# Kernel optimization log

Hardware: AMD Instinct MI355X
Metric: run time of the kernel (lower is better)

The kernel has to match this reference:

```python
import jax, jax.numpy as jnp
import numpy as np

N, E, D, H, ED = 50000, 400000, 64, 4, 16
C = D  # out_channels per head (GATv2Conv(model_dim, model_dim, ...))


def setup_inputs() -> dict:
    key = jax.random.key(0)
    ks = jax.random.split(key, 24)
    sD = 1.0 / np.sqrt(D)
    sE = 1.0 / np.sqrt(ED)
    sC = 1.0 / np.sqrt(C)
    inp = {
        "h": jax.random.normal(ks[0], (N, D), jnp.float32),
        "edge_index": jax.random.randint(ks[1], (2, E), 0, N, dtype=jnp.int32),
        "edge_attr": jax.random.normal(ks[2], (E, ED), jnp.float32),
    }
    for i, name in enumerate(["g1", "g2"]):
        b = 3 + i * 9
        inp[f"{name}_Wl"] = jax.random.normal(ks[b], (D, H * C), jnp.float32) * sD
        inp[f"{name}_bl"] = jax.random.normal(ks[b + 1], (H * C,), jnp.float32) * 0.02
        inp[f"{name}_Wr"] = jax.random.normal(ks[b + 2], (D, H * C), jnp.float32) * sD
        inp[f"{name}_br"] = jax.random.normal(ks[b + 3], (H * C,), jnp.float32) * 0.02
        inp[f"{name}_We"] = jax.random.normal(ks[b + 4], (ED, H * C), jnp.float32) * sE
        inp[f"{name}_att"] = jax.random.normal(ks[b + 5], (H, C), jnp.float32) * sC
        inp[f"{name}_bias"] = jax.random.normal(ks[b + 6], (C,), jnp.float32) * 0.02
        inp[f"ln{i+1}_g"] = jnp.ones((D,), jnp.float32)
        inp[f"ln{i+1}_b"] = jnp.zeros((D,), jnp.float32)
    return inp


def _layer_norm(x, g, b):
    mu = jnp.mean(x, axis=-1, keepdims=True)
    var = jnp.mean((x - mu) ** 2, axis=-1, keepdims=True)
    return (x - mu) * jax.lax.rsqrt(var + 1e-5) * g + b


def _gatv2(h, src, dst, edge_attr, Wl, bl, Wr, br, We, att, bias):
    # PyG GATv2Conv, concat=False, negative_slope=0.2, aggregation at dst
    xl = (h @ Wl + bl).reshape(N, H, C)  # source transform
    xr = (h @ Wr + br).reshape(N, H, C)  # target transform
    ez = (edge_attr @ We).reshape(E, H, C)
    x = jax.nn.leaky_relu(xl[src] + xr[dst] + ez, negative_slope=0.2)  # [E,H,C]
    alpha = jnp.einsum('ehc,hc->eh', x, att)  # attention logits per edge/head
    amax = jax.ops.segment_max(alpha, dst, num_segments=N)
    amax = jnp.where(jnp.isfinite(amax), amax, 0.0)
    ex = jnp.exp(alpha - amax[dst])
    denom = jax.ops.segment_sum(ex, dst, num_segments=N)
    a = ex / (denom[dst] + 1e-16)  # segment softmax over incoming edges
    out = jax.ops.segment_sum(xl[src] * a[..., None], dst, num_segments=N)  # [N,H,C]
    return jnp.mean(out, axis=1) + bias  # concat=False -> head mean, then bias


def reference(h, edge_index, edge_attr,
              g1_Wl, g1_bl, g1_Wr, g1_br, g1_We, g1_att, g1_bias, ln1_g, ln1_b,
              g2_Wl, g2_bl, g2_Wr, g2_br, g2_We, g2_att, g2_bias, ln2_g, ln2_b):
    src, dst = edge_index[0], edge_index[1]
    identity = h
    x = _gatv2(h, src, dst, edge_attr, g1_Wl, g1_bl, g1_Wr, g1_br, g1_We, g1_att, g1_bias)
    x = jax.nn.gelu(_layer_norm(x, ln1_g, ln1_b), approximate=False)
    x = _gatv2(x, src, dst, edge_attr, g2_Wl, g2_bl, g2_Wr, g2_br, g2_We, g2_att, g2_bias)
    x = _layer_norm(x, ln2_g, ln2_b)
    return jax.nn.gelu(x + identity, approximate=False)
```

## Files before the change

### kernel.cpp

```cpp
#include <hip/hip_runtime.h>
#include <math.h>

#define NN  50000
#define EE  400000
#define DD  64
#define HH  4
#define HC  256
#define EDD 16
#define CAPE 96

typedef _Float16 half_t;
typedef _Float16 h2 __attribute__((ext_vector_type(2)));

__device__ __forceinline__ float gelu_exact(float x) {
    return 0.5f * x * (1.0f + erff(x * 0.70710678118654752440f));
}
__device__ __forceinline__ float fast_exp(float x) {
    return __builtin_amdgcn_exp2f(x * 1.44269504088896340736f);
}

template <int CTRL>
__device__ __forceinline__ float dpp_add(float x) {
    const int t = __builtin_amdgcn_update_dpp(0, __float_as_int(x), CTRL, 0xF, 0xF, true);
    return x + __int_as_float(t);
}
__device__ __forceinline__ float row_sum16(float x) {
    x = dpp_add<0x128>(x);
    x = dpp_add<0x124>(x);
    x = dpp_add<0x122>(x);
    x = dpp_add<0x121>(x);
    return x;
}

__global__ void fill_u32(unsigned* __restrict__ p, unsigned v, int n) {
    int i = blockIdx.x * blockDim.x + threadIdx.x;
    int s = gridDim.x * blockDim.x;
    for (; i < n; i += s) p[i] = v;
}

__global__ void hist_k(const int* __restrict__ ei, int* __restrict__ deg) {
    int e = blockIdx.x * 256 + threadIdx.x;
    if (e < EE) atomicAdd(&deg[ei[EE + e]], 1);
}
__global__ void scan1_k(const int* __restrict__ deg, int* __restrict__ rowptr,
                        int* __restrict__ bsum) {
    __shared__ int s[256];
    int t = threadIdx.x, i = blockIdx.x * 256 + t;
    int v = (i < NN) ? deg[i] : 0;
    s[t] = v; __syncthreads();
    for (int o = 1; o < 256; o <<= 1) {
        int u = (t >= o) ? s[t - o] : 0;
        __syncthreads();
        s[t] += u;
        __syncthreads();
    }
    if (i < NN) rowptr[i] = s[t] - v;
    if (t == 255) bsum[blockIdx.x] = s[255];
}
__global__ void scan3_k(int* __restrict__ rowptr, const int* __restrict__ bsum,
                        int* __restrict__ cursor, int nb) {
    __shared__ int s[256];
    int t = threadIdx.x;
    int v = (t < nb) ? bsum[t] : 0;
    s[t] = v; __syncthreads();
    for (int o = 1; o < 256; o <<= 1) {
        int u = (t >= o) ? s[t - o] : 0;
        __syncthreads();
        s[t] += u;
        __syncthreads();
    }
    const int add = (blockIdx.x > 0) ? s[blockIdx.x - 1] : 0;
    int i = blockIdx.x * 256 + t;
    if (i < NN) {
        int r = rowptr[i] + add;
        rowptr[i] = r;
        cursor[i] = r;
    }
    if (i == 0) rowptr[NN] = EE;
}
__global__ void scatter_k(const int* __restrict__ ei, int* __restrict__ cursor,
                          const float* __restrict__ ea,
                          int* __restrict__ srcs, half_t* __restrict__ ea_h) {
    int e = blockIdx.x * 256 + threadIdx.x;
    if (e >= EE) return;
    int dst = ei[EE + e];
    int pos = atomicAdd(&cursor[dst], 1);
    srcs[pos] = ei[e];
    const float* s = ea + (long)e * EDD;
    half_t tmp[EDD];
#pragma unroll
    for (int k = 0; k < EDD; k++) tmp[k] = (half_t)s[k];
    int4* d = (int4*)(ea_h + (long)pos * EDD);
    d[0] = *(const int4*)&tmp[0];
    d[1] = *(const int4*)&tmp[8];
}

__global__ void wrange_k(const int* __restrict__ rowptr, int* __restrict__ wstart,
                         int* __restrict__ srcs, int nw, int cpe) {
    int w = blockIdx.x * 256 + threadIdx.x;
    if (blockIdx.x == 0 && threadIdx.x < 16) srcs[EE + threadIdx.x] = 0;
    if (w > nw) return;
    if (w == nw) { wstart[nw] = NN; return; }
    const int lo = w * cpe;
    int l = 0, r = NN;
    while (l < r) { int m = (l + r) >> 1; if (rowptr[m] >= lo) r = m; else l = m + 1; }
    wstart[w] = l;
}

__global__ __launch_bounds__(256) void gemm_node_lr(
    const float* __restrict__ X,
    const float* __restrict__ Wl, const float* __restrict__ bl,
    const float* __restrict__ Wr, const float* __restrict__ br,
    float* __restrict__ Yl, float* __restrict__ Yr)
{
    __shared__ half_t xs[32][64];
    const int tid  = threadIdx.x;
    const int col  = tid;
    const int base = blockIdx.x * 32;

#pragma unroll
    for (int i = 0; i < 2; i++) {
        const int f   = tid + i * 256;
        const int r   = f >> 4;
        const int row = base + r;
        const int rr  = (row < NN) ? row : (NN - 1);
        const float4 v = *(const float4*)(X + (long)rr * 64 + ((f & 15) << 2));
        h2 p0; p0.x = (half_t)v.x; p0.y = (half_t)v.y;
        h2 p1; p1.x = (half_t)v.z; p1.y = (half_t)v.w;
        int2 w;
        w.x = __builtin_bit_cast(int, p0);
        w.y = __builtin_bit_cast(int, p1);
        *(int2*)&xs[r][(f & 15) << 2] = w;
    }

    int wlp[32], wrp[32];
#pragma unroll
    for (int kk = 0; kk < 32; kk++) {
        h2 a;
        a.x = (half_t)Wl[(2 * kk)     * 256 + col];
        a.y = (half_t)Wl[(2 * kk + 1) * 256 + col];
        wlp[kk] = __builtin_bit_cast(int, a);
        h2 b;
        b.x = (half_t)Wr[(2 * kk)     * 256 + col];
        b.y = (half_t)Wr[(2 * kk + 1) * 256 + col];
        wrp[kk] = __builtin_bit_cast(int, b);
    }
    const float bbl = bl[col];
    const float bbr = br[col];

    __syncthreads();

#pragma unroll 2
    for (int r = 0; r < 32; r++) {
        const int row = base + r;
        float l0 = 0.f, l1 = 0.f, l2 = 0.f, l3 = 0.f;
        float r0 = 0.f, r1 = 0.f, r2 = 0.f, r3 = 0.f;
#pragma unroll
        for (int q = 0; q < 8; q++) {
            const int4 blk = *(const int4*)&xs[r][q << 3];
            const int* pr = (const int*)&blk;
            l0 = __builtin_amdgcn_fdot2(__builtin_bit_cast(h2, pr[0]),
                                        __builtin_bit_cast(h2, wlp[q * 4 + 0]), l0, false);
            l1 = __builtin_amdgcn_fdot2(__builtin_bit_cast(h2, pr[1]),
                                        __builtin_bit_cast(h2, wlp[q * 4 + 1]), l1, false);
            l2 = __builtin_amdgcn_fdot2(__builtin_bit_cast(h2, pr[2]),
                                        __builtin_bit_cast(h2, wlp[q * 4 + 2]), l2, false);
            l3 = __builtin_amdgcn_fdot2(__builtin_bit_cast(h2, pr[3]),
                                        __builtin_bit_cast(h2, wlp[q * 4 + 3]), l3, false);
            r0 = __builtin_amdgcn_fdot2(__builtin_bit_cast(h2, pr[0]),
                                        __builtin_bit_cast(h2, wrp[q * 4 + 0]), r0, false);
            r1 = __builtin_amdgcn_fdot2(__builtin_bit_cast(h2, pr[1]),
                                        __builtin_bit_cast(h2, wrp[q * 4 + 1]), r1, false);
            r2 = __builtin_amdgcn_fdot2(__builtin_bit_cast(h2, pr[2]),
                                        __builtin_bit_cast(h2, wrp[q * 4 + 2]), r2, false);
            r3 = __builtin_amdgcn_fdot2(__builtin_bit_cast(h2, pr[3]),
                                        __builtin_bit_cast(h2, wrp[q * 4 + 3]), r3, false);
        }
        if (row < NN) {
            Yl[(long)row * 256 + col] = (l0 + l1) + (l2 + l3) + bbl;
            Yr[(long)row * 256 + col] = (r0 + r1) + (r2 + r3) + bbr;
        }
    }
}

__device__ __forceinline__ float edge_part_dot2(const h2 ev[8], const int wpk[8][4],
                                                const float4 xlv, const float4 xrv,
                                                const float4 a4) {
    float e0 = 0.f, e1 = 0.f, e2 = 0.f, e3 = 0.f;
#pragma unroll
    for (int k = 0; k < 8; k++) {
        e0 = __builtin_amdgcn_fdot2(ev[k], __builtin_bit_cast(h2, wpk[k][0]), e0, false);
        e1 = __builtin_amdgcn_fdot2(ev[k], __builtin_bit_cast(h2, wpk[k][1]), e1, false);
        e2 = __builtin_amdgcn_fdot2(ev[k], __builtin_bit_cast(h2, wpk[k][2]), e2, false);
        e3 = __builtin_amdgcn_fdot2(ev[k], __builtin_bit_cast(h2, wpk[k][3]), e3, false);
    }
    float s0 = xlv.x + xrv.x + e0;
    float s1 = xlv.y + xrv.y + e1;
    float s2 = xlv.z + xrv.z + e2;
    float s3 = xlv.w + xrv.w + e3;
    s0 = (s0 > 0.f) ? s0 : 0.2f * s0;
    s1 = (s1 > 0.f) ? s1 : 0.2f * s1;
    s2 = (s2 > 0.f) ? s2 : 0.2f * s2;
    s3 = (s3 > 0.f) ? s3 : 0.2f * s3;
    return fmaf(s0, a4.x, fmaf(s1, a4.y, fmaf(s2, a4.z, s3 * a4.w)));
}

__global__ __launch_bounds__(256, 4) void fused_edge_node_k(
    const int* __restrict__ wstart,
    const int* __restrict__ rowptr, const int* __restrict__ srcs,
    const half_t* __restrict__ ea_h,
    const float* __restrict__ We, const float* __restrict__ att,
    const float* __restrict__ xl, const float* __restrict__ xr,
    const float* __restrict__ bias, const float* __restrict__ lng,
    const float* __restrict__ lnb, const float* __restrict__ identity,
    float* __restrict__ x1out, float* __restrict__ outp, int mode)
{
    __shared__ int4 eabuf[4][CAPE * 2];
    const int lane  = threadIdx.x & 63;
    const int wslot = threadIdx.x >> 6;
    const int h     = lane >> 4;
    const int jj    = lane & 15;
    const int gc    = (h << 6) + (jj << 2);
    const int c     = (jj << 2) + h;

    int wpk[8][4];
#pragma unroll
    for (int kk = 0; kk < 8; kk++) {
#pragma unroll
        for (int j = 0; j < 4; j++) {
            h2 t;
            t.x = (half_t)We[(2 * kk)     * HC + gc + j];
            t.y = (half_t)We[(2 * kk + 1) * HC + gc + j];
            wpk[kk][j] = __builtin_bit_cast(int, t);
        }
    }
#pragma unroll
    for (int kk = 0; kk < 8; kk++)
#pragma unroll
        for (int j = 0; j < 4; j++) asm volatile("" : "+v"(wpk[kk][j]));

    const float4 a4 = *(const float4*)(att + gc);
    const float bb  = bias[c];
    const float gg  = lng[c];
    const float cc  = lnb[c];

    const int wid  = blockIdx.x * 4 + wslot;
    const int nbeg = __builtin_amdgcn_readfirstlane(wstart[wid]);
    const int nend = __builtin_amdgcn_readfirstlane(wstart[wid + 1]);

    const int estart = __builtin_amdgcn_readfirstlane(rowptr[nbeg]);
    const int eend   = __builtin_amdgcn_readfirstlane(rowptr[nend]);
    {
        int nstage = eend - estart;
        if (nstage > CAPE) nstage = CAPE;
        const int4* __restrict__ gsrc = (const int4*)(ea_h + (long)estart * EDD);
        int4* l4 = &eabuf[wslot][0];
        for (int i = lane; i < nstage * 2; i += 64) l4[i] = gsrc[i];
    }

    int p0v = rowptr[nbeg];
    int p1v = rowptr[nbeg + 1];
    int sAn = srcs[p0v];
    int sBn = srcs[p0v + 1];

    for (int n = nbeg; n < nend; n++) {
        const int p0 = __builtin_amdgcn_readfirstlane(p0v);
        const int p1 = __builtin_amdgcn_readfirstlane(p1v);
        p0v = p1;
        p1v = rowptr[(n + 2 <= NN) ? (n + 2) : NN];
        int sA = sAn, sB = sBn;
        sAn = srcs[p1];
        sBn = srcs[p1 + 1];

        const float4 xrv = *(const float4*)(xr + (long)n * HC + gc);

        float dsum = 0.f;
        float ac0 = 0.f, ac1 = 0.f, ac2 = 0.f, ac3 = 0.f;

        int p = p0;
        for (; p + 1 < p1; p += 2) {
            const int srcA = __builtin_amdgcn_readfirstlane(sA);
            const int srcB = __builtin_amdgcn_readfirstlane(sB);
            sA = srcs[p + 2];
            sB = srcs[p + 3];

            const float4 xA = *(const float4*)(xl + (long)srcA * HC + gc);
            const float4 xB = *(const float4*)(xl + (long)srcB * HC + gc);

            int idx = p - estart;
            if (idx > CAPE - 2) idx = CAPE - 2;
            const int4* __restrict__ e4 = &eabuf[wslot][idx * 2];
            h2 evA[8], evB[8];
            *(int4*)&evA[0] = e4[0];  *(int4*)&evA[4] = e4[1];
            *(int4*)&evB[0] = e4[2];  *(int4*)&evB[4] = e4[3];

            float ptA = edge_part_dot2(evA, wpk, xA, xrv, a4);
            float ptB = edge_part_dot2(evB, wpk, xB, xrv, a4);

            ptA = row_sum16(ptA);
            ptB = row_sum16(ptB);

            const float wA = fast_exp(ptA);
            const float wB = fast_exp(ptB);
            dsum += (wA + wB);
            ac0 = fmaf(wA, xA.x, ac0); ac1 = fmaf(wA, xA.y, ac1);
            ac2 = fmaf(wA, xA.z, ac2); ac3 = fmaf(wA, xA.w, ac3);
            ac0 = fmaf(wB, xB.x, ac0); ac1 = fmaf(wB, xB.y, ac1);
            ac2 = fmaf(wB, xB.z, ac2); ac3 = fmaf(wB, xB.w, ac3);
        }

        if (p < p1) {
            const int src = __builtin_amdgcn_readfirstlane(sA);
            const float4 xv = *(const float4*)(xl + (long)src * HC + gc);
            int idx = p - estart;
            if (idx > CAPE - 1) idx = CAPE - 1;
            const int4* __restrict__ e4 = &eabuf[wslot][idx * 2];
            h2 ev[8];
            *(int4*)&ev[0] = e4[0];  *(int4*)&ev[4] = e4[1];
            float pt = edge_part_dot2(ev, wpk, xv, xrv, a4);
            pt = row_sum16(pt);
            const float w = fast_exp(pt);
            dsum += w;
            ac0 = fmaf(w, xv.x, ac0); ac1 = fmaf(w, xv.y, ac1);
            ac2 = fmaf(w, xv.z, ac2); ac3 = fmaf(w, xv.w, ac3);
        }

        const float inv = 1.0f / (dsum + 1e-16f);
        float v0 = ac0 * inv, v1 = ac1 * inv, v2 = ac2 * inv, v3 = ac3 * inv;

        v0 += __shfl_xor(v0, 16, 64); v0 += __shfl_xor(v0, 32, 64);
        v1 += __shfl_xor(v1, 16, 64); v1 += __shfl_xor(v1, 32, 64);
        v2 += __shfl_xor(v2, 16, 64); v2 += __shfl_xor(v2, 32, 64);
        v3 += __shfl_xor(v3, 16, 64); v3 += __shfl_xor(v3, 32, 64);

        float vv = (h == 0) ? v0 : (h == 1) ? v1 : (h == 2) ? v2 : v3;
        vv = vv * 0.25f + bb;

        float s = row_sum16(vv);
        s += __shfl_xor(s, 16, 64); s += __shfl_xor(s, 32, 64);
        const float mu = s * (1.0f / 64.0f);
        const float d  = vv - mu;
        float qv = row_sum16(d * d);
        qv += __shfl_xor(qv, 16, 64); qv += __shfl_xor(qv, 32, 64);
        const float rs = rsqrtf(qv * (1.0f / 64.0f) + 1e-5f);

        const float y = d * rs * gg + cc;
        if (mode == 0) {
            x1out[(long)n * DD + c] = gelu_exact(y);
        } else {
            const float id = identity[(long)n * DD + c];
            outp[(long)n * DD + c] = gelu_exact(y + id);
        }
    }
}

extern "C" void kernel_launch(void* const* d_in, const int* in_sizes, int n_in,
                              void* d_out, int out_size, void* d_ws, size_t ws_size,
                              hipStream_t stream) {
    (void)in_sizes; (void)n_in; (void)out_size; (void)ws_size;

    const float* h     = (const float*)d_in[0];
    const int*   ei    = (const int*)d_in[1];
    const float* ea    = (const float*)d_in[2];
    const float* g1Wl  = (const float*)d_in[3];
    const float* g1bl  = (const float*)d_in[4];
    const float* g1Wr  = (const float*)d_in[5];
    const float* g1br  = (const float*)d_in[6];
    const float* g1We  = (const float*)d_in[7];
    const float* g1att = (const float*)d_in[8];
    const float* g1bias= (const float*)d_in[9];
    const float* ln1g  = (const float*)d_in[10];
    const float* ln1b  = (const float*)d_in[11];
    const float* g2Wl  = (const float*)d_in[12];
    const float* g2bl  = (const float*)d_in[13];
    const float* g2Wr  = (const float*)d_in[14];
    const float* g2br  = (const float*)d_in[15];
    const float* g2We  = (const float*)d_in[16];
    const float* g2att = (const float*)d_in[17];
    const float* g2bias= (const float*)d_in[18];
    const float* ln2g  = (const float*)d_in[19];
    const float* ln2b  = (const float*)d_in[20];

    float* out = (float*)d_out;

    const int FUSED_BLOCKS = 4096;
    const int NW  = FUSED_BLOCKS * 4;
    const int CPE = (EE + NW - 1) / NW;

    float* ws = (float*)d_ws;
    size_t o = 0;
    float* xl     = ws + o;         o += 12800000;
    float* xr     = ws + o;         o += 12800000;
    float* x1     = ws + o;         o += 3200000;
    int*   rowptr = (int*)(ws + o); o += 50004;
    int*   deg    = (int*)(ws + o); o += 50000;
    int*   cursor = (int*)(ws + o); o += 50000;
    int*   bsum   = (int*)(ws + o); o += 256;
    int*   srcs   = (int*)(ws + o); o += 400016;
    int*   wstart = (int*)(ws + o); o += NW + 8;
    half_t* ea_h  = (half_t*)(ws + o); o += 3200064;

    const int GEMM_BLOCKS  = (NN + 31) / 32;
    const int SCAN_BLOCKS  = (NN + 255) / 256;
    const int EDGE_BLOCKS  = (EE + 255) / 256;
    const int WR_BLOCKS    = (NW + 1 + 255) / 256;

    fill_u32<<<256, 256, 0, stream>>>((unsigned*)deg, 0u, NN);
    hist_k<<<EDGE_BLOCKS, 256, 0, stream>>>(ei, deg);
    scan1_k<<<SCAN_BLOCKS, 256, 0, stream>>>(deg, rowptr, bsum);
    scan3_k<<<SCAN_BLOCKS, 256, 0, stream>>>(rowptr, bsum, cursor, SCAN_BLOCKS);
    wrange_k<<<WR_BLOCKS, 256, 0, stream>>>(rowptr, wstart, srcs, NW, CPE);
    scatter_k<<<EDGE_BLOCKS, 256, 0, stream>>>(ei, cursor, ea, srcs, ea_h);

    gemm_node_lr<<<GEMM_BLOCKS, 256, 0, stream>>>(h, g1Wl, g1bl, g1Wr, g1br, xl, xr);
    fused_edge_node_k<<<FUSED_BLOCKS, 256, 0, stream>>>(wstart, rowptr, srcs, ea_h,
                                                        g1We, g1att, xl, xr,
                                                        g1bias, ln1g, ln1b,
                                                        h, x1, out, 0);

    gemm_node_lr<<<GEMM_BLOCKS, 256, 0, stream>>>(x1, g2Wl, g2bl, g2Wr, g2br, xl, xr);
    fused_edge_node_k<<<FUSED_BLOCKS, 256, 0, stream>>>(wstart, rowptr, srcs, ea_h,
                                                        g2We, g2att, xl, xr,
                                                        g2bias, ln2g, ln2b,
                                                        h, x1, out, 1);
}
```

Measured before the change: 404.8 us.

## Merge CSR construction kernels into one cooperative kernel with grid syncs

Replaces six separate preprocessing launches (zero-fill, histogram, two scan passes, warp-range search, scatter) with one cooperative kernel of 1024 blocks that uses grid.sync between phases. The wrange search and the scatter now run in the same phase. The goal is to remove per-launch overhead and gaps between the small kernels. The cost is four grid-wide barriers, and the kernel depends on all 1024 blocks being co-resident for the cooperative launch.

```diff
diff --git a/kernel.cpp b/kernel.cpp
--- a/kernel.cpp
+++ b/kernel.cpp
@@ -1,4 +1,5 @@
 #include <hip/hip_runtime.h>
+#include <hip/hip_cooperative_groups.h>
 #include <math.h>
 
 #define NN  50000
@@ -32,79 +33,80 @@
     return x;
 }
 
-__global__ void fill_u32(unsigned* __restrict__ p, unsigned v, int n) {
-    int i = blockIdx.x * blockDim.x + threadIdx.x;
-    int s = gridDim.x * blockDim.x;
-    for (; i < n; i += s) p[i] = v;
-}
-
-__global__ void hist_k(const int* __restrict__ ei, int* __restrict__ deg) {
-    int e = blockIdx.x * 256 + threadIdx.x;
-    if (e < EE) atomicAdd(&deg[ei[EE + e]], 1);
-}
-__global__ void scan1_k(const int* __restrict__ deg, int* __restrict__ rowptr,
-                        int* __restrict__ bsum) {
+__global__ __launch_bounds__(256) void csr_coop_k(
+    const int* __restrict__ ei, const float* __restrict__ ea,
+    int* __restrict__ deg, int* __restrict__ rowptr, int* __restrict__ cursor,
+    int* __restrict__ bsum, int* __restrict__ srcs, half_t* __restrict__ ea_h,
+    int* __restrict__ wstart, int nw, int cpe)
+{
+    cooperative_groups::grid_group grid = cooperative_groups::this_grid();
     __shared__ int s[256];
-    int t = threadIdx.x, i = blockIdx.x * 256 + t;
-    int v = (i < NN) ? deg[i] : 0;
-    s[t] = v; __syncthreads();
-    for (int o = 1; o < 256; o <<= 1) {
-        int u = (t >= o) ? s[t - o] : 0;
-        __syncthreads();
-        s[t] += u;
-        __syncthreads();
-    }
-    if (i < NN) rowptr[i] = s[t] - v;
-    if (t == 255) bsum[blockIdx.x] = s[255];
-}
-__global__ void scan3_k(int* __restrict__ rowptr, const int* __restrict__ bsum,
-                        int* __restrict__ cursor, int nb) {
-    __shared__ int s[256];
-    int t = threadIdx.x;
-    int v = (t < nb) ? bsum[t] : 0;
-    s[t] = v; __syncthreads();
-    for (int o = 1; o < 256; o <<= 1) {
-        int u = (t >= o) ? s[t - o] : 0;
-        __syncthreads();
-        s[t] += u;
-        __syncthreads();
-    }
-    const int add = (blockIdx.x > 0) ? s[blockIdx.x - 1] : 0;
-    int i = blockIdx.x * 256 + t;
-    if (i < NN) {
-        int r = rowptr[i] + add;
-        rowptr[i] = r;
-        cursor[i] = r;
-    }
-    if (i == 0) rowptr[NN] = EE;
-}
-__global__ void scatter_k(const int* __restrict__ ei, int* __restrict__ cursor,
-                          const float* __restrict__ ea,
-                          int* __restrict__ srcs, half_t* __restrict__ ea_h) {
-    int e = blockIdx.x * 256 + threadIdx.x;
-    if (e >= EE) return;
-    int dst = ei[EE + e];
-    int pos = atomicAdd(&cursor[dst], 1);
-    srcs[pos] = ei[e];
-    const float* s = ea + (long)e * EDD;
-    half_t tmp[EDD];
-#pragma unroll
-    for (int k = 0; k < EDD; k++) tmp[k] = (half_t)s[k];
-    int4* d = (int4*)(ea_h + (long)pos * EDD);
-    d[0] = *(const int4*)&tmp[0];
-    d[1] = *(const int4*)&tmp[8];
-}
-
-__global__ void wrange_k(const int* __restrict__ rowptr, int* __restrict__ wstart,
-                         int* __restrict__ srcs, int nw, int cpe) {
-    int w = blockIdx.x * 256 + threadIdx.x;
-    if (blockIdx.x == 0 && threadIdx.x < 16) srcs[EE + threadIdx.x] = 0;
-    if (w > nw) return;
-    if (w == nw) { wstart[nw] = NN; return; }
-    const int lo = w * cpe;
-    int l = 0, r = NN;
-    while (l < r) { int m = (l + r) >> 1; if (rowptr[m] >= lo) r = m; else l = m + 1; }
-    wstart[w] = l;
+    const int tid  = blockIdx.x * 256 + threadIdx.x;
+    const int nthr = gridDim.x * 256;
+    const int nch  = (NN + 255) / 256;
+
+    for (int i = tid; i < NN; i += nthr) deg[i] = 0;
+    grid.sync();
+
+    for (int e = tid; e < EE; e += nthr) atomicAdd(&deg[ei[EE + e]], 1);
+    grid.sync();
+
+    if (blockIdx.x < nch) {
+        const int t = threadIdx.x, i = blockIdx.x * 256 + t;
+        const int v = (i < NN) ? deg[i] : 0;
+        s[t] = v; __syncthreads();
+        for (int o = 1; o < 256; o <<= 1) {
+            int u = (t >= o) ? s[t - o] : 0;
+            __syncthreads();
+            s[t] += u;
+            __syncthreads();
+        }
+        if (i < NN) rowptr[i] = s[t] - v;
+        if (t == 255) bsum[blockIdx.x] = s[255];
+    }
+    grid.sync();
+
+    if (blockIdx.x < nch) {
+        const int t = threadIdx.x;
+        const int v = (t < nch) ? bsum[t] : 0;
+        s[t] = v; __syncthreads();
+        for (int o = 1; o < 256; o <<= 1) {
+            int u = (t >= o) ? s[t - o] : 0;
+            __syncthreads();
+            s[t] += u;
+            __syncthreads();
+        }
+        const int add = (blockIdx.x > 0) ? s[blockIdx.x - 1] : 0;
+        const int i = blockIdx.x * 256 + t;
+        if (i < NN) {
+            const int r = rowptr[i] + add;
+            rowptr[i] = r;
+            cursor[i] = r;
+        }
+        if (i == 0) rowptr[NN] = EE;
+    }
+    grid.sync();
+
+    for (int w = tid; w <= nw; w += nthr) {
+        if (w == nw) { wstart[nw] = NN; continue; }
+        const int lo = w * cpe;
+        int l = 0, r = NN;
+        while (l < r) { int m = (l + r) >> 1; if (rowptr[m] >= lo) r = m; else l = m + 1; }
+        wstart[w] = l;
+    }
+    if (tid < 16) srcs[EE + tid] = 0;
+    for (int e = tid; e < EE; e += nthr) {
+        const int dst = ei[EE + e];
+        const int pos = atomicAdd(&cursor[dst], 1);
+        srcs[pos] = ei[e];
+        const float* sp = ea + (long)e * EDD;
+        half_t tmp[EDD];
+#pragma unroll
+        for (int k = 0; k < EDD; k++) tmp[k] = (half_t)sp[k];
+        int4* d = (int4*)(ea_h + (long)pos * EDD);
+        d[0] = *(const int4*)&tmp[0];
+        d[1] = *(const int4*)&tmp[8];
+    }
 }
 
 __global__ __launch_bounds__(256) void gemm_node_lr(
@@ -400,17 +402,18 @@
     int*   wstart = (int*)(ws + o); o += NW + 8;
     half_t* ea_h  = (half_t*)(ws + o); o += 3200064;
 
-    const int GEMM_BLOCKS  = (NN + 31) / 32;
-    const int SCAN_BLOCKS  = (NN + 255) / 256;
-    const int EDGE_BLOCKS  = (EE + 255) / 256;
-    const int WR_BLOCKS    = (NW + 1 + 255) / 256;
-
-    fill_u32<<<256, 256, 0, stream>>>((unsigned*)deg, 0u, NN);
-    hist_k<<<EDGE_BLOCKS, 256, 0, stream>>>(ei, deg);
-    scan1_k<<<SCAN_BLOCKS, 256, 0, stream>>>(deg, rowptr, bsum);
-    scan3_k<<<SCAN_BLOCKS, 256, 0, stream>>>(rowptr, bsum, cursor, SCAN_BLOCKS);
-    wrange_k<<<WR_BLOCKS, 256, 0, stream>>>(rowptr, wstart, srcs, NW, CPE);
-    scatter_k<<<EDGE_BLOCKS, 256, 0, stream>>>(ei, cursor, ea, srcs, ea_h);
+    const int GEMM_BLOCKS = (NN + 31) / 32;
+
+    {
+        int nwv = NW, cpev = CPE;
+        void* args[] = {
+            (void*)&ei, (void*)&ea, (void*)&deg, (void*)&rowptr,
+            (void*)&cursor, (void*)&bsum, (void*)&srcs, (void*)&ea_h,
+            (void*)&wstart, (void*)&nwv, (void*)&cpev
+        };
+        hipLaunchCooperativeKernel((void*)csr_coop_k, dim3(1024), dim3(256),
+                                   args, 0, stream);
+    }
 
     gemm_node_lr<<<GEMM_BLOCKS, 256, 0, stream>>>(h, g1Wl, g1bl, g1Wr, g1br, xl, xr);
     fused_edge_node_k<<<FUSED_BLOCKS, 256, 0, stream>>>(wstart, rowptr, srcs, ea_h,
```

New measurement: 790.5 us. 1.95x slower.
